# Kernel tuning notes

Hardware: AMD Instinct MI355X
Metric: run time of the kernel (lower is better)

The kernel has to match this reference:

```python
import jax, jax.numpy as jnp
import numpy as np

NEG_INF = -1e30


def setup_inputs() -> dict:
    key = jax.random.key(0)
    kq, kk, kv, ks = jax.random.split(key, 4)
    B, H, S, D = 2, 16, 2048, 64
    return {
        "q": jax.random.normal(kq, (B, H, S, D), dtype=jnp.float32),
        "k": jax.random.normal(kk, (B, H, S, D), dtype=jnp.float32),
        "v": jax.random.normal(kv, (B, H, S, D), dtype=jnp.float32),
        "sink_weights": jax.random.normal(ks, (H,), dtype=jnp.float32),
        "sliding_window": 1024,
    }


def reference(q, k, v, sink_weights, sliding_window):
    """Sliding-window causal attention with a learnable attention-sink logit.

    Equivalent to FlexAttention.forward with sink_weights given: an extra kv
    position (the sink) is appended whose score is replaced by sink_weights[h]
    and whose value is zero -> it only adds mass to the softmax denominator.
    """
    B, H, S_q, D = q.shape
    S_kv = k.shape[2]
    scale = 1.0 / np.sqrt(D)

    # [B, H, S_q, S_kv] raw scores
    scores = jnp.einsum("bhqd,bhkd->bhqk", q, k) * scale

    q_idx = jnp.arange(S_q)[:, None]
    kv_idx = jnp.arange(S_kv)[None, :]
    keep = (kv_idx <= q_idx) & (q_idx - kv_idx <= sliding_window)  # [S_q, S_kv]
    scores = jnp.where(keep[None, None], scores, NEG_INF)

    # sink column: per-head learnable logit, always visible
    sink_col = jnp.broadcast_to(
        sink_weights[None, :, None, None], (B, H, S_q, 1)
    )
    logits = jnp.concatenate([scores, sink_col], axis=-1)  # [B,H,S_q,S_kv+1]

    probs = jax.nn.softmax(logits, axis=-1)
    # sink value is zero, so only the first S_kv prob columns hit v
    out = jnp.einsum("bhqk,bhkd->bhqd", probs[..., :S_kv], v)
    return out
```

## Files before the change

### kernel.cpp

```cpp
#include <hip/hip_runtime.h>


typedef __bf16 bf16x8 __attribute__((ext_vector_type(8)));
typedef __bf16 bf16x4 __attribute__((ext_vector_type(4)));
typedef float  f32x16 __attribute__((ext_vector_type(16)));

#define NT 256
#define NEG_BIG (-3.0e38f)

__device__ __forceinline__ int swz(int row, int gran) {
    return row * 64 + ((gran ^ ((row >> 1) & 7)) << 3);
}

__device__ __forceinline__ void plswap(unsigned &a, unsigned &b) {
    asm("v_permlane32_swap_b32 %0, %1" : "+v"(a), "+v"(b));
}

__device__ __forceinline__ float xmax32(float x) {
    float a = x, b;
    asm("v_mov_b32 %0, %1" : "=&v"(b) : "v"(a));
    asm("v_permlane32_swap_b32 %0, %1" : "+v"(a), "+v"(b));
    return fmaxf(a, b);
}

__device__ __forceinline__ float xsum32(float x) {
    float a = x, b;
    asm("v_mov_b32 %0, %1" : "=&v"(b) : "v"(a));
    asm("v_permlane32_swap_b32 %0, %1" : "+v"(a), "+v"(b));
    return a + b;
}

__device__ const int SEG_N[24] = {3,2,2,2,2,1,2,1, 1,1,1,1,1,1,1,1, 1,1,1,1,1,1,1,1};
__device__ const int SEG_IT[24][3] = {
  {0,1,2},{2,3,0},{3,4,0},{4,5,0},{5,6,0},{6,0,0},{6,7,0},{7,0,0},
  {8,0,0},{8,0,0},{9,0,0},{9,0,0},{10,0,0},{10,0,0},{11,0,0},{11,0,0},
  {12,0,0},{12,0,0},{13,0,0},{13,0,0},{14,0,0},{14,0,0},{15,0,0},{15,0,0}};
__device__ const int SEG_J0[24][3] = {
  {0,0,0},{3,0,0},{6,0,0},{7,0,0},{6,0,0},{3,0,0},{12,0,0},{7,0,0},
  {0,0,0},{9,0,0},{0,0,0},{9,0,0},{0,0,0},{9,0,0},{0,0,0},{9,0,0},
  {0,0,0},{9,0,0},{0,0,0},{9,0,0},{0,0,0},{9,0,0},{0,0,0},{9,0,0}};
__device__ const int SEG_J1[24][3] = {
  {2,4,3},{6,6,0},{8,7,0},{10,6,0},{12,3,0},{12,0,0},{14,7,0},{16,0,0},
  {9,0,0},{18,0,0},{9,0,0},{18,0,0},{9,0,0},{18,0,0},{9,0,0},{18,0,0},
  {9,0,0},{18,0,0},{9,0,0},{18,0,0},{9,0,0},{18,0,0},{9,0,0},{18,0,0}};
__device__ const int SEG_SX[24][3] = {
  {0,0,0},{1,0,0},{1,0,0},{1,0,0},{1,0,0},{1,0,0},{2,0,0},{1,0,0},
  {0,0,0},{1,0,0},{0,0,0},{1,0,0},{0,0,0},{1,0,0},{0,0,0},{1,0,0},
  {0,0,0},{1,0,0},{0,0,0},{1,0,0},{0,0,0},{1,0,0},{0,0,0},{1,0,0}};
__device__ const int NSEG_ITEM[16] = {1,1,2,2,2,2,3,2, 2,2,2,2,2,2,2,2};

__global__ __launch_bounds__(NT, 3) void flex_r16_main(
    const float* __restrict__ Q, const float* __restrict__ K,
    const float* __restrict__ V, const float* __restrict__ SINKW,
    const int* __restrict__ SWIN, void* __restrict__ WS,
    float* __restrict__ OUT, const int H, const int S)
{
    const int t    = threadIdx.x;
    const int lane = t & 63;
    const int w    = t >> 6;
    const int c    = lane & 31;
    const int hl   = lane >> 5;
    const int W    = SWIN[0];
    const float scale = 0.125f;

    const int NBH = gridDim.x / 24;
    int bh, b24;
    if ((NBH & 7) == 0) {
        const int xcd  = blockIdx.x & 7;
        const int rest = blockIdx.x >> 3;
        const int G    = NBH >> 3;
        bh  = (rest % G) * 8 + xcd;
        b24 = rest / G;
    } else {
        bh  = blockIdx.x / 24;
        b24 = blockIdx.x - bh * 24;
    }
    const int h   = bh % H;
    const float sw = SINKW[h];

    __shared__ __align__(16) __bf16 k_lds[2][64 * 64];
    __shared__ __align__(16) __bf16 v_lds[2][64 * 64];

    const size_t basebh = (size_t)bh * S * 64;
    const float4* kp4 = (const float4*)(K + basebh);
    const float4* vp4 = (const float4*)(V + basebh);
    __bf16* O_ws  = (__bf16*)WS;
    float2* ml_ws = (float2*)((char*)WS + (size_t)NBH * 48 * 16384);

    const int dgi = t & 15;
    const int kgi = t >> 4;
    float4 kreg[4], vreg[4];

    const int ns = SEG_N[b24];

    {
        const int it0 = SEG_IT[b24][0];
        const int ktA0 = (2 * it0 - 16 > 0) ? (2 * it0 - 16) : 0;
        const int kt = ktA0 + SEG_J0[b24][0];
        #pragma unroll
        for (int i = 0; i < 4; ++i) kreg[i] = kp4[kt * 1024 + i * NT + t];
        #pragma unroll
        for (int kk = 0; kk < 4; ++kk) vreg[kk] = vp4[kt * 1024 + (4 * kgi + kk) * 16 + dgi];
        #pragma unroll
        for (int i = 0; i < 4; ++i) {
            const int flat = i * NT + t;
            const int key = flat >> 4, dd = flat & 15;
            float4 f = kreg[i];
            bf16x4 b = { (__bf16)f.x, (__bf16)f.y, (__bf16)f.z, (__bf16)f.w };
            *(bf16x4*)&k_lds[0][swz(key, dd >> 1) + (dd & 1) * 4] = b;
        }
        {
            float4 a0 = vreg[0], a1 = vreg[1], a2 = vreg[2], a3 = vreg[3];
            bf16x4 w0 = { (__bf16)a0.x, (__bf16)a1.x, (__bf16)a2.x, (__bf16)a3.x };
            bf16x4 w1 = { (__bf16)a0.y, (__bf16)a1.y, (__bf16)a2.y, (__bf16)a3.y };
            bf16x4 w2 = { (__bf16)a0.z, (__bf16)a1.z, (__bf16)a2.z, (__bf16)a3.z };
            bf16x4 w3 = { (__bf16)a0.w, (__bf16)a1.w, (__bf16)a2.w, (__bf16)a3.w };
            const int gv = kgi >> 1, ov = (kgi & 1) * 4;
            *(bf16x4*)&v_lds[0][swz(4 * dgi + 0, gv) + ov] = w0;
            *(bf16x4*)&v_lds[0][swz(4 * dgi + 1, gv) + ov] = w1;
            *(bf16x4*)&v_lds[0][swz(4 * dgi + 2, gv) + ov] = w2;
            *(bf16x4*)&v_lds[0][swz(4 * dgi + 3, gv) + ov] = w3;
        }
    }

    int par = 0;

    for (int s = 0; s < ns; ++s) {
        const int item = SEG_IT[b24][s];
        const int j0   = SEG_J0[b24][s];
        const int j1   = SEG_J1[b24][s];
        const int sidx = SEG_SX[b24][s];
        const int ktA  = (2 * item - 16 > 0) ? (2 * item - 16) : 0;
        const int qw0  = item * 128 + 32 * w;
        const int qi   = qw0 + c;

        bf16x8 bq[4];
        {
            const float4* qp4 = (const float4*)(Q + basebh + (size_t)qi * 64);
            #pragma unroll
            for (int ks = 0; ks < 4; ++ks) {
                float4 f0 = qp4[4 * ks + 2 * hl];
                float4 f1 = qp4[4 * ks + 2 * hl + 1];
                bq[ks][0] = (__bf16)(f0.x * scale); bq[ks][1] = (__bf16)(f0.y * scale);
                bq[ks][2] = (__bf16)(f0.z * scale); bq[ks][3] = (__bf16)(f0.w * scale);
                bq[ks][4] = (__bf16)(f1.x * scale); bq[ks][5] = (__bf16)(f1.y * scale);
                bq[ks][6] = (__bf16)(f1.z * scale); bq[ks][7] = (__bf16)(f1.w * scale);
            }
        }

        float mrun = (sidx == 0) ? sw : NEG_BIG;
        float lrun = (sidx == 0) ? 1.0f : 0.0f;
        f32x16 accO0, accO1;
        #pragma unroll
        for (int i = 0; i < 16; ++i) { accO0[i] = 0.0f; accO1[i] = 0.0f; }

        for (int j = j0; j < j1; ++j) {
            const int k0 = (ktA + j) * 64;

            __syncthreads();

            int nkt = -1;
            if (j + 1 < j1) nkt = ktA + j + 1;
            else if (s + 1 < ns) {
                const int it2 = SEG_IT[b24][s + 1];
                const int ktA2 = (2 * it2 - 16 > 0) ? (2 * it2 - 16) : 0;
                nkt = ktA2 + SEG_J0[b24][s + 1];
            }
            if (nkt >= 0) {
                #pragma unroll
                for (int i = 0; i < 4; ++i) kreg[i] = kp4[nkt * 1024 + i * NT + t];
                #pragma unroll
                for (int kk = 0; kk < 4; ++kk) vreg[kk] = vp4[nkt * 1024 + (4 * kgi + kk) * 16 + dgi];
            }

            const __bf16* kb = k_lds[par];
            const __bf16* vb = v_lds[par];
            f32x16 accS0, accS1;
            #pragma unroll
            for (int i = 0; i < 16; ++i) { accS0[i] = 0.0f; accS1[i] = 0.0f; }
            __builtin_amdgcn_s_setprio(1);
            #pragma unroll
            for (int ks = 0; ks < 4; ++ks) {
                bf16x8 ka0 = *(const bf16x8*)&kb[swz(c,      2 * ks + hl)];
                bf16x8 ka1 = *(const bf16x8*)&kb[swz(32 + c, 2 * ks + hl)];
                accS0 = __builtin_amdgcn_mfma_f32_32x32x16_bf16(ka0, bq[ks], accS0, 0, 0, 0);
                accS1 = __builtin_amdgcn_mfma_f32_32x32x16_bf16(ka1, bq[ks], accS1, 0, 0, 0);
            }
            __builtin_amdgcn_s_setprio(0);

            const bool interior = (k0 + 63 <= qw0) && (qw0 + 31 - k0 <= W);
            if (!interior) {
                #pragma unroll
                for (int rg = 0; rg < 16; ++rg) {
                    const int kb2 = (rg & 3) + 8 * (rg >> 2) + 4 * hl;
                    const int ki0 = k0 + kb2, ki1 = k0 + 32 + kb2;
                    if (!((ki0 <= qi) && (qi - ki0 <= W))) accS0[rg] = -1e30f;
                    if (!((ki1 <= qi) && (qi - ki1 <= W))) accS1[rg] = -1e30f;
                }
            }

            float q4[8];
            #pragma unroll
            for (int i = 0; i < 4; ++i) {
                q4[i]   = fmaxf(fmaxf(accS0[4*i], accS0[4*i+1]),
                                fmaxf(accS0[4*i+2], accS0[4*i+3]));
                q4[4+i] = fmaxf(fmaxf(accS1[4*i], accS1[4*i+1]),
                                fmaxf(accS1[4*i+2], accS1[4*i+3]));
            }
            float mx = fmaxf(fmaxf(fmaxf(q4[0], q4[1]), fmaxf(q4[2], q4[3])),
                             fmaxf(fmaxf(q4[4], q4[5]), fmaxf(q4[6], q4[7])));
            mx = xmax32(mx);
            if (!__all(mx <= mrun + 8.0f)) {
                const float mnew  = fmaxf(mrun, mx);
                const float alpha = __expf(mrun - mnew);
                lrun *= alpha;
                #pragma unroll
                for (int i = 0; i < 16; ++i) { accO0[i] *= alpha; accO1[i] *= alpha; }
                mrun = mnew;
            }
            float ps = 0.0f;
            #pragma unroll
            for (int i = 0; i < 16; ++i) { float p = __expf(accS0[i] - mrun); accS0[i] = p; ps += p; }
            #pragma unroll
            for (int i = 0; i < 16; ++i) { float p = __expf(accS1[i] - mrun); accS1[i] = p; ps += p; }
            ps = xsum32(ps);
            lrun += ps;

            union B4U { bf16x4 v; unsigned u[2]; };
            B4U a0, b0, a1, b1, a2, b2, a3, b3;
            a0.v = bf16x4{ (__bf16)accS0[0],  (__bf16)accS0[1],  (__bf16)accS0[2],  (__bf16)accS0[3]  };
            b0.v = bf16x4{ (__bf16)accS0[4],  (__bf16)accS0[5],  (__bf16)accS0[6],  (__bf16)accS0[7]  };
            a1.v = bf16x4{ (__bf16)accS0[8],  (__bf16)accS0[9],  (__bf16)accS0[10], (__bf16)accS0[11] };
            b1.v = bf16x4{ (__bf16)accS0[12], (__bf16)accS0[13], (__bf16)accS0[14], (__bf16)accS0[15] };
            a2.v = bf16x4{ (__bf16)accS1[0],  (__bf16)accS1[1],  (__bf16)accS1[2],  (__bf16)accS1[3]  };
            b2.v = bf16x4{ (__bf16)accS1[4],  (__bf16)accS1[5],  (__bf16)accS1[6],  (__bf16)accS1[7]  };
            a3.v = bf16x4{ (__bf16)accS1[8],  (__bf16)accS1[9],  (__bf16)accS1[10], (__bf16)accS1[11] };
            b3.v = bf16x4{ (__bf16)accS1[12], (__bf16)accS1[13], (__bf16)accS1[14], (__bf16)accS1[15] };
            plswap(a0.u[0], b0.u[0]); plswap(a0.u[1], b0.u[1]);
            plswap(a1.u[0], b1.u[0]); plswap(a1.u[1], b1.u[1]);
            plswap(a2.u[0], b2.u[0]); plswap(a2.u[1], b2.u[1]);
            plswap(a3.u[0], b3.u[0]); plswap(a3.u[1], b3.u[1]);
            bf16x8 bp[4];
            #pragma unroll
            for (int e = 0; e < 4; ++e) {
                bp[0][e] = a0.v[e]; bp[0][4+e] = b0.v[e];
                bp[1][e] = a1.v[e]; bp[1][4+e] = b1.v[e];
                bp[2][e] = a2.v[e]; bp[2][4+e] = b2.v[e];
                bp[3][e] = a3.v[e]; bp[3][4+e] = b3.v[e];
            }

            __builtin_amdgcn_s_setprio(1);
            #pragma unroll
            for (int ks = 0; ks < 4; ++ks) {
                bf16x8 va0 = *(const bf16x8*)&vb[swz(c,      2 * ks + hl)];
                bf16x8 va1 = *(const bf16x8*)&vb[swz(32 + c, 2 * ks + hl)];
                accO0 = __builtin_amdgcn_mfma_f32_32x32x16_bf16(va0, bp[ks], accO0, 0, 0, 0);
                accO1 = __builtin_amdgcn_mfma_f32_32x32x16_bf16(va1, bp[ks], accO1, 0, 0, 0);
            }
            __builtin_amdgcn_s_setprio(0);

            if (nkt >= 0) {
                const int np = par ^ 1;
                #pragma unroll
                for (int i = 0; i < 4; ++i) {
                    const int flat = i * NT + t;
                    const int key = flat >> 4, dd = flat & 15;
                    float4 f = kreg[i];
                    bf16x4 b = { (__bf16)f.x, (__bf16)f.y, (__bf16)f.z, (__bf16)f.w };
                    *(bf16x4*)&k_lds[np][swz(key, dd >> 1) + (dd & 1) * 4] = b;
                }
                float4 a0v = vreg[0], a1v = vreg[1], a2v = vreg[2], a3v = vreg[3];
                bf16x4 w0 = { (__bf16)a0v.x, (__bf16)a1v.x, (__bf16)a2v.x, (__bf16)a3v.x };
                bf16x4 w1 = { (__bf16)a0v.y, (__bf16)a1v.y, (__bf16)a2v.y, (__bf16)a3v.y };
                bf16x4 w2 = { (__bf16)a0v.z, (__bf16)a1v.z, (__bf16)a2v.z, (__bf16)a3v.z };
                bf16x4 w3 = { (__bf16)a0v.w, (__bf16)a1v.w, (__bf16)a2v.w, (__bf16)a3v.w };
                const int gv = kgi >> 1, ov = (kgi & 1) * 4;
                *(bf16x4*)&v_lds[np][swz(4 * dgi + 0, gv) + ov] = w0;
                *(bf16x4*)&v_lds[np][swz(4 * dgi + 1, gv) + ov] = w1;
                *(bf16x4*)&v_lds[np][swz(4 * dgi + 2, gv) + ov] = w2;
                *(bf16x4*)&v_lds[np][swz(4 * dgi + 3, gv) + ov] = w3;
            }
            par ^= 1;
        }

        if (item < 2) {
            const float inv = 1.0f / lrun;
            float* ob = OUT + basebh + (size_t)qi * 64;
            #pragma unroll
            for (int rg = 0; rg < 4; ++rg) {
                float4 f0 = { accO0[4*rg+0]*inv, accO0[4*rg+1]*inv,
                              accO0[4*rg+2]*inv, accO0[4*rg+3]*inv };
                float4 f1 = { accO1[4*rg+0]*inv, accO1[4*rg+1]*inv,
                              accO1[4*rg+2]*inv, accO1[4*rg+3]*inv };
                *(float4*)&ob[     8 * rg + 4 * hl] = f0;
                *(float4*)&ob[32 + 8 * rg + 4 * hl] = f1;
            }
        } else {
            const int slot = (bh * 16 + item) * 3 + sidx;
            const int qrel = 32 * w + c;
            if (hl == 0) ml_ws[(size_t)slot * 128 + qrel] = make_float2(mrun, lrun);
            __bf16* Os = O_ws + (size_t)slot * 8192 + (size_t)qrel * 64;
            #pragma unroll
            for (int qd = 0; qd < 4; ++qd) {
                const int d0 = 8 * qd + 4 * hl;
                bf16x4 b0 = { (__bf16)accO0[4*qd+0], (__bf16)accO0[4*qd+1],
                              (__bf16)accO0[4*qd+2], (__bf16)accO0[4*qd+3] };
                bf16x4 b1 = { (__bf16)accO1[4*qd+0], (__bf16)accO1[4*qd+1],
                              (__bf16)accO1[4*qd+2], (__bf16)accO1[4*qd+3] };
                *(bf16x4*)&Os[d0]      = b0;
                *(bf16x4*)&Os[32 + d0] = b1;
            }
        }
    }
}

__global__ __launch_bounds__(256) void flex_r16_combine(
    const void* __restrict__ WS, float* __restrict__ OUT, const int H, const int S)
{
    const int NBH  = gridDim.x / 14;
    const int bi   = blockIdx.x;
    const int bh   = bi / 14;
    const int item = 2 + (bi - bh * 14);
    const int ns   = NSEG_ITEM[item];
    const int t    = threadIdx.x;
    const int q    = t >> 1;
    const int half = t & 1;

    const __bf16* O_ws = (const __bf16*)WS;
    const float2* ml_ws = (const float2*)((const char*)WS + (size_t)NBH * 48 * 16384);
    const int base = (bh * 16 + item) * 3;

    float m[3], lv[3], a[3];
    float mst = NEG_BIG;
    for (int s = 0; s < ns; ++s) {
        float2 e = ml_ws[(size_t)(base + s) * 128 + q];
        m[s] = e.x; lv[s] = e.y;
        mst = fmaxf(mst, m[s]);
    }
    float lst = 0.0f;
    for (int s = 0; s < ns; ++s) { a[s] = __expf(m[s] - mst); lst += a[s] * lv[s]; }
    const float inv = 1.0f / lst;

    float acc[32];
    #pragma unroll
    for (int i = 0; i < 32; ++i) acc[i] = 0.0f;
    for (int s = 0; s < ns; ++s) {
        const __bf16* Os = O_ws + (size_t)(base + s) * 8192 + (size_t)q * 64 + 32 * half;
        const float as = a[s];
        #pragma unroll
        for (int v8 = 0; v8 < 4; ++v8) {
            bf16x8 o = *(const bf16x8*)&Os[8 * v8];
            #pragma unroll
            for (int jj = 0; jj < 8; ++jj) acc[8 * v8 + jj] += as * (float)o[jj];
        }
    }

    float* dst = OUT + (size_t)bh * S * 64 + (size_t)(item * 128 + q) * 64 + 32 * half;
    #pragma unroll
    for (int v4 = 0; v4 < 8; ++v4) {
        float4 f = { acc[4*v4+0] * inv, acc[4*v4+1] * inv,
                     acc[4*v4+2] * inv, acc[4*v4+3] * inv };
        *(float4*)&dst[4 * v4] = f;
    }
}

extern "C" void kernel_launch(void* const* d_in, const int* in_sizes, int n_in,
                              void* d_out, int out_size, void* d_ws, size_t ws_size,
                              hipStream_t stream) {
    const float* q     = (const float*)d_in[0];
    const float* k     = (const float*)d_in[1];
    const float* v     = (const float*)d_in[2];
    const float* sinkw = (const float*)d_in[3];
    const int*   swin  = (const int*)d_in[4];
    float* out = (float*)d_out;

    const int H = in_sizes[3];
    const int S = 2048;
    const int B = in_sizes[0] / (H * S * 64);
    const int NBH = B * H;

    flex_r16_main<<<dim3(NBH * 24), NT, 0, stream>>>(q, k, v, sinkw, swin, d_ws, out, H, S);
    flex_r16_combine<<<dim3(NBH * 14), 256, 0, stream>>>(d_ws, out, H, S);
}
```

Measured before the change: 130.2 us.

## Give each wave 64 query rows with 128-thread blocks and exp2 softmax

The block drops from four waves to two, and each wave now computes two 32-row query tiles against the same K/V fragments read from shared memory, so every LDS read feeds twice as many MFMAs. Scores are pre-scaled by log2(e) so the softmax can use exp2f, and the lazy-rescale threshold rises from 8 to 11 in log2 units. The prefetch of the next K/V tile now starts after the softmax instead of before the QK matmul, and each thread loads 8 float4s. In exchange, register pressure roughly doubles, occupancy drops to two blocks per CU, and fewer waves are available to hide latency.

```diff
diff --git a/kernel.cpp b/kernel.cpp
--- a/kernel.cpp
+++ b/kernel.cpp
@@ -5,8 +5,9 @@
 typedef __bf16 bf16x4 __attribute__((ext_vector_type(4)));
 typedef float  f32x16 __attribute__((ext_vector_type(16)));
 
-#define NT 256
+#define NT 128
 #define NEG_BIG (-3.0e38f)
+#define LOG2E 1.44269504088896f
 
 __device__ __forceinline__ int swz(int row, int gran) {
     return row * 64 + ((gran ^ ((row >> 1) & 7)) << 3);
@@ -28,6 +29,53 @@
     asm("v_mov_b32 %0, %1" : "=&v"(b) : "v"(a));
     asm("v_permlane32_swap_b32 %0, %1" : "+v"(a), "+v"(b));
     return a + b;
+}
+
+__device__ __forceinline__ void exch_bp(const f32x16& sa, const f32x16& sb,
+                                        bf16x8 bp[4]) {
+    union B4U { bf16x4 v; unsigned u[2]; };
+    B4U a0, b0, a1, b1, a2, b2, a3, b3;
+    a0.v = bf16x4{ (__bf16)sa[0],  (__bf16)sa[1],  (__bf16)sa[2],  (__bf16)sa[3]  };
+    b0.v = bf16x4{ (__bf16)sa[4],  (__bf16)sa[5],  (__bf16)sa[6],  (__bf16)sa[7]  };
+    a1.v = bf16x4{ (__bf16)sa[8],  (__bf16)sa[9],  (__bf16)sa[10], (__bf16)sa[11] };
+    b1.v = bf16x4{ (__bf16)sa[12], (__bf16)sa[13], (__bf16)sa[14], (__bf16)sa[15] };
+    a2.v = bf16x4{ (__bf16)sb[0],  (__bf16)sb[1],  (__bf16)sb[2],  (__bf16)sb[3]  };
+    b2.v = bf16x4{ (__bf16)sb[4],  (__bf16)sb[5],  (__bf16)sb[6],  (__bf16)sb[7]  };
+    a3.v = bf16x4{ (__bf16)sb[8],  (__bf16)sb[9],  (__bf16)sb[10], (__bf16)sb[11] };
+    b3.v = bf16x4{ (__bf16)sb[12], (__bf16)sb[13], (__bf16)sb[14], (__bf16)sb[15] };
+    plswap(a0.u[0], b0.u[0]); plswap(a0.u[1], b0.u[1]);
+    plswap(a1.u[0], b1.u[0]); plswap(a1.u[1], b1.u[1]);
+    plswap(a2.u[0], b2.u[0]); plswap(a2.u[1], b2.u[1]);
+    plswap(a3.u[0], b3.u[0]); plswap(a3.u[1], b3.u[1]);
+    #pragma unroll
+    for (int e = 0; e < 4; ++e) {
+        bp[0][e] = a0.v[e]; bp[0][4+e] = b0.v[e];
+        bp[1][e] = a1.v[e]; bp[1][4+e] = b1.v[e];
+        bp[2][e] = a2.v[e]; bp[2][4+e] = b2.v[e];
+        bp[3][e] = a3.v[e]; bp[3][4+e] = b3.v[e];
+    }
+}
+
+__device__ __forceinline__ void mask_half(f32x16& s0, f32x16& s1,
+                                          int k0, int qi, int W, int hl) {
+    #pragma unroll
+    for (int rg = 0; rg < 16; ++rg) {
+        const int kb2 = (rg & 3) + 8 * (rg >> 2) + 4 * hl;
+        const int ki0 = k0 + kb2, ki1 = k0 + 32 + kb2;
+        if (!((ki0 <= qi) && (qi - ki0 <= W))) s0[rg] = -1e30f;
+        if (!((ki1 <= qi) && (qi - ki1 <= W))) s1[rg] = -1e30f;
+    }
+}
+
+__device__ __forceinline__ float tree_max(const f32x16& s0, const f32x16& s1) {
+    float q4[8];
+    #pragma unroll
+    for (int i = 0; i < 4; ++i) {
+        q4[i]   = fmaxf(fmaxf(s0[4*i], s0[4*i+1]), fmaxf(s0[4*i+2], s0[4*i+3]));
+        q4[4+i] = fmaxf(fmaxf(s1[4*i], s1[4*i+1]), fmaxf(s1[4*i+2], s1[4*i+3]));
+    }
+    return fmaxf(fmaxf(fmaxf(q4[0], q4[1]), fmaxf(q4[2], q4[3])),
+                 fmaxf(fmaxf(q4[4], q4[5]), fmaxf(q4[6], q4[7])));
 }
 
 __device__ const int SEG_N[24] = {3,2,2,2,2,1,2,1, 1,1,1,1,1,1,1,1, 1,1,1,1,1,1,1,1};
@@ -49,7 +97,7 @@
   {0,0,0},{1,0,0},{0,0,0},{1,0,0},{0,0,0},{1,0,0},{0,0,0},{1,0,0}};
 __device__ const int NSEG_ITEM[16] = {1,1,2,2,2,2,3,2, 2,2,2,2,2,2,2,2};
 
-__global__ __launch_bounds__(NT, 3) void flex_r16_main(
+__global__ __launch_bounds__(NT, 2) void flex_r17_main(
     const float* __restrict__ Q, const float* __restrict__ K,
     const float* __restrict__ V, const float* __restrict__ SINKW,
     const int* __restrict__ SWIN, void* __restrict__ WS,
@@ -61,7 +109,7 @@
     const int c    = lane & 31;
     const int hl   = lane >> 5;
     const int W    = SWIN[0];
-    const float scale = 0.125f;
+    const float scale = 0.125f * LOG2E;
 
     const int NBH = gridDim.x / 24;
     int bh, b24;
@@ -76,7 +124,7 @@
         b24 = blockIdx.x - bh * 24;
     }
     const int h   = bh % H;
-    const float sw = SINKW[h];
+    const float sw = SINKW[h] * LOG2E;
 
     __shared__ __align__(16) __bf16 k_lds[2][64 * 64];
     __shared__ __align__(16) __bf16 v_lds[2][64 * 64];
@@ -88,8 +136,8 @@
     float2* ml_ws = (float2*)((char*)WS + (size_t)NBH * 48 * 16384);
 
     const int dgi = t & 15;
-    const int kgi = t >> 4;
-    float4 kreg[4], vreg[4];
+    const int kg  = t >> 4;
+    float4 kreg[8], vreg[8];
 
     const int ns = SEG_N[b24];
 
@@ -98,11 +146,11 @@
         const int ktA0 = (2 * it0 - 16 > 0) ? (2 * it0 - 16) : 0;
         const int kt = ktA0 + SEG_J0[b24][0];
         #pragma unroll
-        for (int i = 0; i < 4; ++i) kreg[i] = kp4[kt * 1024 + i * NT + t];
+        for (int i = 0; i < 8; ++i) kreg[i] = kp4[kt * 1024 + i * NT + t];
         #pragma unroll
-        for (int kk = 0; kk < 4; ++kk) vreg[kk] = vp4[kt * 1024 + (4 * kgi + kk) * 16 + dgi];
+        for (int kk = 0; kk < 8; ++kk) vreg[kk] = vp4[kt * 1024 + (8 * kg + kk) * 16 + dgi];
         #pragma unroll
-        for (int i = 0; i < 4; ++i) {
+        for (int i = 0; i < 8; ++i) {
             const int flat = i * NT + t;
             const int key = flat >> 4, dd = flat & 15;
             float4 f = kreg[i];
@@ -110,16 +158,23 @@
             *(bf16x4*)&k_lds[0][swz(key, dd >> 1) + (dd & 1) * 4] = b;
         }
         {
-            float4 a0 = vreg[0], a1 = vreg[1], a2 = vreg[2], a3 = vreg[3];
-            bf16x4 w0 = { (__bf16)a0.x, (__bf16)a1.x, (__bf16)a2.x, (__bf16)a3.x };
-            bf16x4 w1 = { (__bf16)a0.y, (__bf16)a1.y, (__bf16)a2.y, (__bf16)a3.y };
-            bf16x4 w2 = { (__bf16)a0.z, (__bf16)a1.z, (__bf16)a2.z, (__bf16)a3.z };
-            bf16x4 w3 = { (__bf16)a0.w, (__bf16)a1.w, (__bf16)a2.w, (__bf16)a3.w };
-            const int gv = kgi >> 1, ov = (kgi & 1) * 4;
-            *(bf16x4*)&v_lds[0][swz(4 * dgi + 0, gv) + ov] = w0;
-            *(bf16x4*)&v_lds[0][swz(4 * dgi + 1, gv) + ov] = w1;
-            *(bf16x4*)&v_lds[0][swz(4 * dgi + 2, gv) + ov] = w2;
-            *(bf16x4*)&v_lds[0][swz(4 * dgi + 3, gv) + ov] = w3;
+            bf16x4 p0, p1;
+            p0 = bf16x4{ (__bf16)vreg[0].x, (__bf16)vreg[1].x, (__bf16)vreg[2].x, (__bf16)vreg[3].x };
+            p1 = bf16x4{ (__bf16)vreg[4].x, (__bf16)vreg[5].x, (__bf16)vreg[6].x, (__bf16)vreg[7].x };
+            *(bf16x4*)&v_lds[0][swz(4 * dgi + 0, kg) + 0] = p0;
+            *(bf16x4*)&v_lds[0][swz(4 * dgi + 0, kg) + 4] = p1;
+            p0 = bf16x4{ (__bf16)vreg[0].y, (__bf16)vreg[1].y, (__bf16)vreg[2].y, (__bf16)vreg[3].y };
+            p1 = bf16x4{ (__bf16)vreg[4].y, (__bf16)vreg[5].y, (__bf16)vreg[6].y, (__bf16)vreg[7].y };
+            *(bf16x4*)&v_lds[0][swz(4 * dgi + 1, kg) + 0] = p0;
+            *(bf16x4*)&v_lds[0][swz(4 * dgi + 1, kg) + 4] = p1;
+            p0 = bf16x4{ (__bf16)vreg[0].z, (__bf16)vreg[1].z, (__bf16)vreg[2].z, (__bf16)vreg[3].z };
+            p1 = bf16x4{ (__bf16)vreg[4].z, (__bf16)vreg[5].z, (__bf16)vreg[6].z, (__bf16)vreg[7].z };
+            *(bf16x4*)&v_lds[0][swz(4 * dgi + 2, kg) + 0] = p0;
+            *(bf16x4*)&v_lds[0][swz(4 * dgi + 2, kg) + 4] = p1;
+            p0 = bf16x4{ (__bf16)vreg[0].w, (__bf16)vreg[1].w, (__bf16)vreg[2].w, (__bf16)vreg[3].w };
+            p1 = bf16x4{ (__bf16)vreg[4].w, (__bf16)vreg[5].w, (__bf16)vreg[6].w, (__bf16)vreg[7].w };
+            *(bf16x4*)&v_lds[0][swz(4 * dgi + 3, kg) + 0] = p0;
+            *(bf16x4*)&v_lds[0][swz(4 * dgi + 3, kg) + 4] = p1;
         }
     }
 
@@ -131,28 +186,38 @@
         const int j1   = SEG_J1[b24][s];
         const int sidx = SEG_SX[b24][s];
         const int ktA  = (2 * item - 16 > 0) ? (2 * item - 16) : 0;
-        const int qw0  = item * 128 + 32 * w;
-        const int qi   = qw0 + c;
-
-        bf16x8 bq[4];
+        const int qw0  = item * 128 + 64 * w;
+        const int qi0  = qw0 + c;
+        const int qi1  = qw0 + 32 + c;
+
+        bf16x8 bq0[4], bq1[4];
         {
-            const float4* qp4 = (const float4*)(Q + basebh + (size_t)qi * 64);
+            const float4* qpa = (const float4*)(Q + basebh + (size_t)qi0 * 64);
+            const float4* qpb = (const float4*)(Q + basebh + (size_t)qi1 * 64);
             #pragma unroll
             for (int ks = 0; ks < 4; ++ks) {
-                float4 f0 = qp4[4 * ks + 2 * hl];
-                float4 f1 = qp4[4 * ks + 2 * hl + 1];
-                bq[ks][0] = (__bf16)(f0.x * scale); bq[ks][1] = (__bf16)(f0.y * scale);
-                bq[ks][2] = (__bf16)(f0.z * scale); bq[ks][3] = (__bf16)(f0.w * scale);
-                bq[ks][4] = (__bf16)(f1.x * scale); bq[ks][5] = (__bf16)(f1.y * scale);
-                bq[ks][6] = (__bf16)(f1.z * scale); bq[ks][7] = (__bf16)(f1.w * scale);
-            }
-        }
-
-        float mrun = (sidx == 0) ? sw : NEG_BIG;
-        float lrun = (sidx == 0) ? 1.0f : 0.0f;
-        f32x16 accO0, accO1;
+                float4 f0 = qpa[4 * ks + 2 * hl];
+                float4 f1 = qpa[4 * ks + 2 * hl + 1];
+                bq0[ks][0] = (__bf16)(f0.x * scale); bq0[ks][1] = (__bf16)(f0.y * scale);
+                bq0[ks][2] = (__bf16)(f0.z * scale); bq0[ks][3] = (__bf16)(f0.w * scale);
+                bq0[ks][4] = (__bf16)(f1.x * scale); bq0[ks][5] = (__bf16)(f1.y * scale);
+                bq0[ks][6] = (__bf16)(f1.z * scale); bq0[ks][7] = (__bf16)(f1.w * scale);
+                float4 g0 = qpb[4 * ks + 2 * hl];
+                float4 g1 = qpb[4 * ks + 2 * hl + 1];
+                bq1[ks][0] = (__bf16)(g0.x * scale); bq1[ks][1] = (__bf16)(g0.y * scale);
+                bq1[ks][2] = (__bf16)(g0.z * scale); bq1[ks][3] = (__bf16)(g0.w * scale);
+                bq1[ks][4] = (__bf16)(g1.x * scale); bq1[ks][5] = (__bf16)(g1.y * scale);
+                bq1[ks][6] = (__bf16)(g1.z * scale); bq1[ks][7] = (__bf16)(g1.w * scale);
+            }
+        }
+
+        float mrun0 = (sidx == 0) ? sw : NEG_BIG;
+        float mrun1 = mrun0;
+        float lrun0 = (sidx == 0) ? 1.0f : 0.0f;
+        float lrun1 = lrun0;
+        f32x16 o00, o10, o01, o11;
         #pragma unroll
-        for (int i = 0; i < 16; ++i) { accO0[i] = 0.0f; accO1[i] = 0.0f; }
+        for (int i = 0; i < 16; ++i) { o00[i] = 0.0f; o10[i] = 0.0f; o01[i] = 0.0f; o11[i] = 0.0f; }
 
         for (int j = j0; j < j1; ++j) {
             const int k0 = (ktA + j) * 64;
@@ -166,87 +231,66 @@
                 const int ktA2 = (2 * it2 - 16 > 0) ? (2 * it2 - 16) : 0;
                 nkt = ktA2 + SEG_J0[b24][s + 1];
             }
-            if (nkt >= 0) {
-                #pragma unroll
-                for (int i = 0; i < 4; ++i) kreg[i] = kp4[nkt * 1024 + i * NT + t];
-                #pragma unroll
-                for (int kk = 0; kk < 4; ++kk) vreg[kk] = vp4[nkt * 1024 + (4 * kgi + kk) * 16 + dgi];
-            }
 
             const __bf16* kb = k_lds[par];
             const __bf16* vb = v_lds[par];
-            f32x16 accS0, accS1;
-            #pragma unroll
-            for (int i = 0; i < 16; ++i) { accS0[i] = 0.0f; accS1[i] = 0.0f; }
+            f32x16 s00, s10, s01, s11;
+            #pragma unroll
+            for (int i = 0; i < 16; ++i) { s00[i] = 0.0f; s10[i] = 0.0f; s01[i] = 0.0f; s11[i] = 0.0f; }
             __builtin_amdgcn_s_setprio(1);
             #pragma unroll
             for (int ks = 0; ks < 4; ++ks) {
                 bf16x8 ka0 = *(const bf16x8*)&kb[swz(c,      2 * ks + hl)];
                 bf16x8 ka1 = *(const bf16x8*)&kb[swz(32 + c, 2 * ks + hl)];
-                accS0 = __builtin_amdgcn_mfma_f32_32x32x16_bf16(ka0, bq[ks], accS0, 0, 0, 0);
-                accS1 = __builtin_amdgcn_mfma_f32_32x32x16_bf16(ka1, bq[ks], accS1, 0, 0, 0);
+                s00 = __builtin_amdgcn_mfma_f32_32x32x16_bf16(ka0, bq0[ks], s00, 0, 0, 0);
+                s10 = __builtin_amdgcn_mfma_f32_32x32x16_bf16(ka1, bq0[ks], s10, 0, 0, 0);
+                s01 = __builtin_amdgcn_mfma_f32_32x32x16_bf16(ka0, bq1[ks], s01, 0, 0, 0);
+                s11 = __builtin_amdgcn_mfma_f32_32x32x16_bf16(ka1, bq1[ks], s11, 0, 0, 0);
             }
             __builtin_amdgcn_s_setprio(0);
 
-            const bool interior = (k0 + 63 <= qw0) && (qw0 + 31 - k0 <= W);
+            const bool interior = (k0 + 63 <= qw0) && (qw0 + 63 - k0 <= W);
             if (!interior) {
+                mask_half(s00, s10, k0, qi0, W, hl);
+                mask_half(s01, s11, k0, qi1, W, hl);
+            }
+
+            float mx0 = xmax32(tree_max(s00, s10));
+            float mx1 = xmax32(tree_max(s01, s11));
+            if (!__all(fmaxf(mx0 - mrun0, mx1 - mrun1) <= 11.0f)) {
+                const float mn0 = fmaxf(mrun0, mx0);
+                const float al0 = exp2f(mrun0 - mn0);
+                const float mn1 = fmaxf(mrun1, mx1);
+                const float al1 = exp2f(mrun1 - mn1);
+                lrun0 *= al0; lrun1 *= al1;
                 #pragma unroll
-                for (int rg = 0; rg < 16; ++rg) {
-                    const int kb2 = (rg & 3) + 8 * (rg >> 2) + 4 * hl;
-                    const int ki0 = k0 + kb2, ki1 = k0 + 32 + kb2;
-                    if (!((ki0 <= qi) && (qi - ki0 <= W))) accS0[rg] = -1e30f;
-                    if (!((ki1 <= qi) && (qi - ki1 <= W))) accS1[rg] = -1e30f;
+                for (int i = 0; i < 16; ++i) {
+                    o00[i] *= al0; o10[i] *= al0;
+                    o01[i] *= al1; o11[i] *= al1;
                 }
-            }
-
-            float q4[8];
-            #pragma unroll
-            for (int i = 0; i < 4; ++i) {
-                q4[i]   = fmaxf(fmaxf(accS0[4*i], accS0[4*i+1]),
-                                fmaxf(accS0[4*i+2], accS0[4*i+3]));
-                q4[4+i] = fmaxf(fmaxf(accS1[4*i], accS1[4*i+1]),
-                                fmaxf(accS1[4*i+2], accS1[4*i+3]));
-            }
-            float mx = fmaxf(fmaxf(fmaxf(q4[0], q4[1]), fmaxf(q4[2], q4[3])),
-                             fmaxf(fmaxf(q4[4], q4[5]), fmaxf(q4[6], q4[7])));
-            mx = xmax32(mx);
-            if (!__all(mx <= mrun + 8.0f)) {
-                const float mnew  = fmaxf(mrun, mx);
-                const float alpha = __expf(mrun - mnew);
-                lrun *= alpha;
+                mrun0 = mn0; mrun1 = mn1;
+            }
+            float ps0 = 0.0f, ps1 = 0.0f;
+            #pragma unroll
+            for (int i = 0; i < 16; ++i) {
+                float p; 
+                p = exp2f(s00[i] - mrun0); s00[i] = p; ps0 += p;
+                p = exp2f(s10[i] - mrun0); s10[i] = p; ps0 += p;
+                p = exp2f(s01[i] - mrun1); s01[i] = p; ps1 += p;
+                p = exp2f(s11[i] - mrun1); s11[i] = p; ps1 += p;
+            }
+            lrun0 += xsum32(ps0);
+            lrun1 += xsum32(ps1);
+
+            bf16x8 bp0[4], bp1[4];
+            exch_bp(s00, s10, bp0);
+            exch_bp(s01, s11, bp1);
+
+            if (nkt >= 0) {
                 #pragma unroll
-                for (int i = 0; i < 16; ++i) { accO0[i] *= alpha; accO1[i] *= alpha; }
-                mrun = mnew;
-            }
-            float ps = 0.0f;
-            #pragma unroll
-            for (int i = 0; i < 16; ++i) { float p = __expf(accS0[i] - mrun); accS0[i] = p; ps += p; }
-            #pragma unroll
-            for (int i = 0; i < 16; ++i) { float p = __expf(accS1[i] - mrun); accS1[i] = p; ps += p; }
-            ps = xsum32(ps);
-            lrun += ps;
-
-            union B4U { bf16x4 v; unsigned u[2]; };
-            B4U a0, b0, a1, b1, a2, b2, a3, b3;
-            a0.v = bf16x4{ (__bf16)accS0[0],  (__bf16)accS0[1],  (__bf16)accS0[2],  (__bf16)accS0[3]  };
-            b0.v = bf16x4{ (__bf16)accS0[4],  (__bf16)accS0[5],  (__bf16)accS0[6],  (__bf16)accS0[7]  };
-            a1.v = bf16x4{ (__bf16)accS0[8],  (__bf16)accS0[9],  (__bf16)accS0[10], (__bf16)accS0[11] };
-            b1.v = bf16x4{ (__bf16)accS0[12], (__bf16)accS0[13], (__bf16)accS0[14], (__bf16)accS0[15] };
-            a2.v = bf16x4{ (__bf16)accS1[0],  (__bf16)accS1[1],  (__bf16)accS1[2],  (__bf16)accS1[3]  };
-            b2.v = bf16x4{ (__bf16)accS1[4],  (__bf16)accS1[5],  (__bf16)accS1[6],  (__bf16)accS1[7]  };
-            a3.v = bf16x4{ (__bf16)accS1[8],  (__bf16)accS1[9],  (__bf16)accS1[10], (__bf16)accS1[11] };
-            b3.v = bf16x4{ (__bf16)accS1[12], (__bf16)accS1[13], (__bf16)accS1[14], (__bf16)accS1[15] };
-            plswap(a0.u[0], b0.u[0]); plswap(a0.u[1], b0.u[1]);
-            plswap(a1.u[0], b1.u[0]); plswap(a1.u[1], b1.u[1]);
-            plswap(a2.u[0], b2.u[0]); plswap(a2.u[1], b2.u[1]);
-            plswap(a3.u[0], b3.u[0]); plswap(a3.u[1], b3.u[1]);
-            bf16x8 bp[4];
-            #pragma unroll
-            for (int e = 0; e < 4; ++e) {
-                bp[0][e] = a0.v[e]; bp[0][4+e] = b0.v[e];
-                bp[1][e] = a1.v[e]; bp[1][4+e] = b1.v[e];
-                bp[2][e] = a2.v[e]; bp[2][4+e] = b2.v[e];
-                bp[3][e] = a3.v[e]; bp[3][4+e] = b3.v[e];
+                for (int i = 0; i < 8; ++i) kreg[i] = kp4[nkt * 1024 + i * NT + t];
+                #pragma unroll
+                for (int kk = 0; kk < 8; ++kk) vreg[kk] = vp4[nkt * 1024 + (8 * kg + kk) * 16 + dgi];
             }
 
             __builtin_amdgcn_s_setprio(1);
@@ -254,67 +298,87 @@
             for (int ks = 0; ks < 4; ++ks) {
                 bf16x8 va0 = *(const bf16x8*)&vb[swz(c,      2 * ks + hl)];
                 bf16x8 va1 = *(const bf16x8*)&vb[swz(32 + c, 2 * ks + hl)];
-                accO0 = __builtin_amdgcn_mfma_f32_32x32x16_bf16(va0, bp[ks], accO0, 0, 0, 0);
-                accO1 = __builtin_amdgcn_mfma_f32_32x32x16_bf16(va1, bp[ks], accO1, 0, 0, 0);
+                o00 = __builtin_amdgcn_mfma_f32_32x32x16_bf16(va0, bp0[ks], o00, 0, 0, 0);
+                o10 = __builtin_amdgcn_mfma_f32_32x32x16_bf16(va1, bp0[ks], o10, 0, 0, 0);
+                o01 = __builtin_amdgcn_mfma_f32_32x32x16_bf16(va0, bp1[ks], o01, 0, 0, 0);
+                o11 = __builtin_amdgcn_mfma_f32_32x32x16_bf16(va1, bp1[ks], o11, 0, 0, 0);
             }
             __builtin_amdgcn_s_setprio(0);
 
             if (nkt >= 0) {
                 const int np = par ^ 1;
                 #pragma unroll
-                for (int i = 0; i < 4; ++i) {
+                for (int i = 0; i < 8; ++i) {
                     const int flat = i * NT + t;
                     const int key = flat >> 4, dd = flat & 15;
                     float4 f = kreg[i];
                     bf16x4 b = { (__bf16)f.x, (__bf16)f.y, (__bf16)f.z, (__bf16)f.w };
                     *(bf16x4*)&k_lds[np][swz(key, dd >> 1) + (dd & 1) * 4] = b;
                 }
-                float4 a0v = vreg[0], a1v = vreg[1], a2v = vreg[2], a3v = vreg[3];
-                bf16x4 w0 = { (__bf16)a0v.x, (__bf16)a1v.x, (__bf16)a2v.x, (__bf16)a3v.x };
-                bf16x4 w1 = { (__bf16)a0v.y, (__bf16)a1v.y, (__bf16)a2v.y, (__bf16)a3v.y };
-                bf16x4 w2 = { (__bf16)a0v.z, (__bf16)a1v.z, (__bf16)a2v.z, (__bf16)a3v.z };
-                bf16x4 w3 = { (__bf16)a0v.w, (__bf16)a1v.w, (__bf16)a2v.w, (__bf16)a3v.w };
-                const int gv = kgi >> 1, ov = (kgi & 1) * 4;
-                *(bf16x4*)&v_lds[np][swz(4 * dgi + 0, gv) + ov] = w0;
-                *(bf16x4*)&v_lds[np][swz(4 * dgi + 1, gv) + ov] = w1;
-                *(bf16x4*)&v_lds[np][swz(4 * dgi + 2, gv) + ov] = w2;
-                *(bf16x4*)&v_lds[np][swz(4 * dgi + 3, gv) + ov] = w3;
+                bf16x4 p0, p1;
+                p0 = bf16x4{ (__bf16)vreg[0].x, (__bf16)vreg[1].x, (__bf16)vreg[2].x, (__bf16)vreg[3].x };
+                p1 = bf16x4{ (__bf16)vreg[4].x, (__bf16)vreg[5].x, (__bf16)vreg[6].x, (__bf16)vreg[7].x };
+                *(bf16x4*)&v_lds[np][swz(4 * dgi + 0, kg) + 0] = p0;
+                *(bf16x4*)&v_lds[np][swz(4 * dgi + 0, kg) + 4] = p1;
+                p0 = bf16x4{ (__bf16)vreg[0].y, (__bf16)vreg[1].y, (__bf16)vreg[2].y, (__bf16)vreg[3].y };
+                p1 = bf16x4{ (__bf16)vreg[4].y, (__bf16)vreg[5].y, (__bf16)vreg[6].y, (__bf16)vreg[7].y };
+                *(bf16x4*)&v_lds[np][swz(4 * dgi + 1, kg) + 0] = p0;
+                *(bf16x4*)&v_lds[np][swz(4 * dgi + 1, kg) + 4] = p1;
+                p0 = bf16x4{ (__bf16)vreg[0].z, (__bf16)vreg[1].z, (__bf16)vreg[2].z, (__bf16)vreg[3].z };
+                p1 = bf16x4{ (__bf16)vreg[4].z, (__bf16)vreg[5].z, (__bf16)vreg[6].z, (__bf16)vreg[7].z };
+                *(bf16x4*)&v_lds[np][swz(4 * dgi + 2, kg) + 0] = p0;
+                *(bf16x4*)&v_lds[np][swz(4 * dgi + 2, kg) + 4] = p1;
+                p0 = bf16x4{ (__bf16)vreg[0].w, (__bf16)vreg[1].w, (__bf16)vreg[2].w, (__bf16)vreg[3].w };
+                p1 = bf16x4{ (__bf16)vreg[4].w, (__bf16)vreg[5].w, (__bf16)vreg[6].w, (__bf16)vreg[7].w };
+                *(bf16x4*)&v_lds[np][swz(4 * dgi + 3, kg) + 0] = p0;
+                *(bf16x4*)&v_lds[np][swz(4 * dgi + 3, kg) + 4] = p1;
             }
             par ^= 1;
         }
 
         if (item < 2) {
-            const float inv = 1.0f / lrun;
-            float* ob = OUT + basebh + (size_t)qi * 64;
+            const float inv0 = 1.0f / lrun0;
+            const float inv1 = 1.0f / lrun1;
+            float* ob0 = OUT + basebh + (size_t)qi0 * 64;
+            float* ob1 = OUT + basebh + (size_t)qi1 * 64;
             #pragma unroll
             for (int rg = 0; rg < 4; ++rg) {
-                float4 f0 = { accO0[4*rg+0]*inv, accO0[4*rg+1]*inv,
-                              accO0[4*rg+2]*inv, accO0[4*rg+3]*inv };
-                float4 f1 = { accO1[4*rg+0]*inv, accO1[4*rg+1]*inv,
-                              accO1[4*rg+2]*inv, accO1[4*rg+3]*inv };
-                *(float4*)&ob[     8 * rg + 4 * hl] = f0;
-                *(float4*)&ob[32 + 8 * rg + 4 * hl] = f1;
+                float4 f0 = { o00[4*rg+0]*inv0, o00[4*rg+1]*inv0, o00[4*rg+2]*inv0, o00[4*rg+3]*inv0 };
+                float4 f1 = { o10[4*rg+0]*inv0, o10[4*rg+1]*inv0, o10[4*rg+2]*inv0, o10[4*rg+3]*inv0 };
+                *(float4*)&ob0[     8 * rg + 4 * hl] = f0;
+                *(float4*)&ob0[32 + 8 * rg + 4 * hl] = f1;
+                float4 g0 = { o01[4*rg+0]*inv1, o01[4*rg+1]*inv1, o01[4*rg+2]*inv1, o01[4*rg+3]*inv1 };
+                float4 g1 = { o11[4*rg+0]*inv1, o11[4*rg+1]*inv1, o11[4*rg+2]*inv1, o11[4*rg+3]*inv1 };
+                *(float4*)&ob1[     8 * rg + 4 * hl] = g0;
+                *(float4*)&ob1[32 + 8 * rg + 4 * hl] = g1;
             }
         } else {
             const int slot = (bh * 16 + item) * 3 + sidx;
-            const int qrel = 32 * w + c;
-            if (hl == 0) ml_ws[(size_t)slot * 128 + qrel] = make_float2(mrun, lrun);
-            __bf16* Os = O_ws + (size_t)slot * 8192 + (size_t)qrel * 64;
+            const int qr0 = 64 * w + c;
+            const int qr1 = 64 * w + 32 + c;
+            if (hl == 0) {
+                ml_ws[(size_t)slot * 128 + qr0] = make_float2(mrun0, lrun0);
+                ml_ws[(size_t)slot * 128 + qr1] = make_float2(mrun1, lrun1);
+            }
+            __bf16* Os0 = O_ws + (size_t)slot * 8192 + (size_t)qr0 * 64;
+            __bf16* Os1 = O_ws + (size_t)slot * 8192 + (size_t)qr1 * 64;
             #pragma unroll
             for (int qd = 0; qd < 4; ++qd) {
                 const int d0 = 8 * qd + 4 * hl;
-                bf16x4 b0 = { (__bf16)accO0[4*qd+0], (__bf16)accO0[4*qd+1],
-                              (__bf16)accO0[4*qd+2], (__bf16)accO0[4*qd+3] };
-                bf16x4 b1 = { (__bf16)accO1[4*qd+0], (__bf16)accO1[4*qd+1],
-                              (__bf16)accO1[4*qd+2], (__bf16)accO1[4*qd+3] };
-                *(bf16x4*)&Os[d0]      = b0;
-                *(bf16x4*)&Os[32 + d0] = b1;
-            }
-        }
-    }
-}
-
-__global__ __launch_bounds__(256) void flex_r16_combine(
+                bf16x4 b0 = { (__bf16)o00[4*qd+0], (__bf16)o00[4*qd+1], (__bf16)o00[4*qd+2], (__bf16)o00[4*qd+3] };
+                bf16x4 b1 = { (__bf16)o10[4*qd+0], (__bf16)o10[4*qd+1], (__bf16)o10[4*qd+2], (__bf16)o10[4*qd+3] };
+                *(bf16x4*)&Os0[d0]      = b0;
+                *(bf16x4*)&Os0[32 + d0] = b1;
+                bf16x4 c0 = { (__bf16)o01[4*qd+0], (__bf16)o01[4*qd+1], (__bf16)o01[4*qd+2], (__bf16)o01[4*qd+3] };
+                bf16x4 c1 = { (__bf16)o11[4*qd+0], (__bf16)o11[4*qd+1], (__bf16)o11[4*qd+2], (__bf16)o11[4*qd+3] };
+                *(bf16x4*)&Os1[d0]      = c0;
+                *(bf16x4*)&Os1[32 + d0] = c1;
+            }
+        }
+    }
+}
+
+__global__ __launch_bounds__(256) void flex_r17_combine(
     const void* __restrict__ WS, float* __restrict__ OUT, const int H, const int S)
 {
     const int NBH  = gridDim.x / 14;
@@ -338,7 +402,7 @@
         mst = fmaxf(mst, m[s]);
     }
     float lst = 0.0f;
-    for (int s = 0; s < ns; ++s) { a[s] = __expf(m[s] - mst); lst += a[s] * lv[s]; }
+    for (int s = 0; s < ns; ++s) { a[s] = exp2f(m[s] - mst); lst += a[s] * lv[s]; }
     const float inv = 1.0f / lst;
 
     float acc[32];
@@ -379,6 +443,6 @@
     const int B = in_sizes[0] / (H * S * 64);
     const int NBH = B * H;
 
-    flex_r16_main<<<dim3(NBH * 24), NT, 0, stream>>>(q, k, v, sinkw, swin, d_ws, out, H, S);
-    flex_r16_combine<<<dim3(NBH * 14), 256, 0, stream>>>(d_ws, out, H, S);
-}
+    flex_r17_main<<<dim3(NBH * 24), NT, 0, stream>>>(q, k, v, sinkw, swin, d_ws, out, H, S);
+    flex_r17_combine<<<dim3(NBH * 14), 256, 0, stream>>>(d_ws, out, H, S);
+}
```

Measured after the change: 169.3 us. +30.0%, slower.
